# Kernel tuning notes

Hardware: AMD Instinct MI355X
Metric: run time of the kernel (lower is better)

## Reference

```python
import jax, jax.numpy as jnp
import numpy as np

TIME_STEPS = 49      # time_steps init arg
NUM_STEPS = 5000     # (time_steps+1)/dt = max_solve_steps
DT = 0.01            # dt0 in diffeqsolve
B = 8192             # batch of independent simulations


def setup_inputs() -> dict:
    key = jax.random.key(0)
    k1, k2, k3 = jax.random.split(key, 3)
    # positive, well-conditioned rates in [0.05, 0.5)
    condition = 0.05 + 0.45 * jax.random.uniform(k1, (B, 4), dtype=jnp.float32)
    # standard normals; scaled by sqrt(dt) inside reference -> Brownian increments
    dW = jax.random.normal(k2, (NUM_STEPS, B), dtype=jnp.float32)
    # uniform jitter used in summarize()'s max_at
    u = jax.random.uniform(k3, (B,), dtype=jnp.float32)
    return {"condition": condition, "dW": dW, "u": u}


def _simulate(condition, dW):
    # condition columns: infection_rate, recovery_rate, r0_mean_reversion, r0_volatility
    inf_rate = condition[:, 0]
    rec = condition[:, 1]
    mr = condition[:, 2]
    vol = condition[:, 3]
    r0_init = inf_rate / rec
    b = condition.shape[0]
    y0 = jnp.stack([
        jnp.full((b,), 0.99, condition.dtype),  # S
        jnp.full((b,), 0.01, condition.dtype),  # I
        jnp.zeros((b,), condition.dtype),       # R
        r0_init,                                # R0
    ], axis=-1)  # [B,4]
    sqrt_dt = jnp.sqrt(jnp.asarray(DT, condition.dtype))

    def step(y, dw):
        s, i, r, r0 = y[:, 0], y[:, 1], y[:, 2], y[:, 3]
        newly_infected = r0 * rec * s
        newly_recovered = rec * i
        # Euler-Maruyama: drift * dt + diffusion * dW, diffusion only on R0,
        # scaled by sqrt(|R0|) as in sde()
        y_new = jnp.stack([
            s - DT * newly_infected,
            i + DT * (newly_infected - newly_recovered),
            r + DT * newly_recovered,
            r0 + DT * mr * (r0_init - r0) + jnp.sqrt(jnp.abs(r0)) * vol * (dw * sqrt_dt),
        ], axis=-1)
        return y_new, y_new[:, 1]  # carry full state, emit infected fraction

    _, infected = jax.lax.scan(step, y0, dW)  # infected: [NUM_STEPS, B]
    # SaveAt ts = 1..TIME_STEPS: step k ends at t=(k+1)*DT, so t=m is index 100*m-1
    x = infected[99:100 * TIME_STEPS:100]  # [TIME_STEPS, B]
    return jnp.nan_to_num(x, nan=0.0, posinf=0.0, neginf=0.0)


def reference(condition, dW, u):
    x = _simulate(condition, dW)          # [T, B] infected trajectories
    x = jnp.clip(x, 1e-5)
    max_ = x.max(axis=0)
    max_at = (jnp.argmax(x, axis=0).astype(x.dtype) + u) / TIME_STEPS
    vol = jnp.std(jnp.diff(jnp.log(x), axis=0), axis=0)
    return jnp.stack([max_, max_at, vol], axis=-1)  # [B, 3]
```

## Files before the change

kernel.cpp:

```cpp
#include <hip/hip_runtime.h>
#include <math.h>

#define BATCH 8192
#define TPB   32
#define SLOT  100
#define NSLOT 49
#define RING  3
#define SLOT_BYTES  (SLOT * TPB * 4)
#define GROUP_BYTES (10 * TPB * 4)


__device__ __forceinline__ unsigned lds_addr_of(void* p) {
    return (unsigned)(unsigned long long)(__attribute__((address_space(3))) void*)p;
}

#define REP10(M) M(0) M(1) M(2) M(3) M(4) M(5) M(6) M(7) M(8) M(9)

#define DECLA(k) float A##k = 0.0f;
#define DECLB(k) float B##k = 0.0f;

#define DS_READ10(P, addr) asm volatile( \
    "ds_read_b32 %[d0], %[a] offset:0\n\t" \
    "ds_read_b32 %[d1], %[a] offset:128\n\t" \
    "ds_read_b32 %[d2], %[a] offset:256\n\t" \
    "ds_read_b32 %[d3], %[a] offset:384\n\t" \
    "ds_read_b32 %[d4], %[a] offset:512\n\t" \
    "ds_read_b32 %[d5], %[a] offset:640\n\t" \
    "ds_read_b32 %[d6], %[a] offset:768\n\t" \
    "ds_read_b32 %[d7], %[a] offset:896\n\t" \
    "ds_read_b32 %[d8], %[a] offset:1024\n\t" \
    "ds_read_b32 %[d9], %[a] offset:1152" \
    : [d0] "=v"(P##0), [d1] "=v"(P##1), [d2] "=v"(P##2), [d3] "=v"(P##3), \
      [d4] "=v"(P##4), [d5] "=v"(P##5), [d6] "=v"(P##6), [d7] "=v"(P##7), \
      [d8] "=v"(P##8), [d9] "=v"(P##9) \
    : [a] "v"(addr))

#define WAIT10(P) asm volatile("s_waitcnt lgkmcnt(10)" \
    : "+v"(P##0), "+v"(P##1), "+v"(P##2), "+v"(P##3), "+v"(P##4), \
      "+v"(P##5), "+v"(P##6), "+v"(P##7), "+v"(P##8), "+v"(P##9))

#define WAIT10_0(P) asm volatile("s_waitcnt lgkmcnt(0)" \
    : "+v"(P##0), "+v"(P##1), "+v"(P##2), "+v"(P##3), "+v"(P##4), \
      "+v"(P##5), "+v"(P##6), "+v"(P##7), "+v"(P##8), "+v"(P##9))

#define STEP_BODY(dwv) { \
    float dw  = (dwv); \
    float pr  = dtrec * r0; \
    float ps  = pr * s; \
    float r0a = r0 * c1 + c2; \
    float sq  = sqrtf(fabsf(r0)); \
    float g   = dw * volc; \
    s  = s - ps; \
    i_ = i_ * ci + ps; \
    r0 = r0a + sq * g; }

#define STEPA(k) STEP_BODY(A##k)
#define STEPB(k) STEP_BODY(B##k)

#define ISSUE_SLOT(kk) do { \
    const float* g_ = gp + (size_t)(kk) * (SLOT * BATCH); \
    float* l_ = &ring[(kk) % RING][0][0]; \
    _Pragma("unroll") \
    for (int ii = 0; ii < 25; ++ii) { \
        __builtin_amdgcn_global_load_lds( \
            (__attribute__((address_space(1))) void*)(g_), \
            (__attribute__((address_space(3))) void*)(l_), 16, 0, 0); \
        g_ += 4 * BATCH; \
        l_ += 4 * TPB; \
    } \
} while (0)

__global__ __launch_bounds__(TPB, 1)
void sir_sde_kernel(const float* __restrict__ cond,
                    const float* __restrict__ dW,
                    const float* __restrict__ uu,
                    float* __restrict__ out)
{
    __shared__ float ring[RING][SLOT][TPB];

    const int t = threadIdx.x;
    const int b = blockIdx.x * TPB + t;
    const int b0 = blockIdx.x * TPB;

    const float inf_rate = cond[b * 4 + 0];
    const float rec      = cond[b * 4 + 1];
    const float mr       = cond[b * 4 + 2];
    const float vol      = cond[b * 4 + 3];
    const float u        = uu[b];

    const float dt    = 0.01f;
    const float r0i   = inf_rate / rec;
    const float dtrec = dt * rec;
    const float ci    = 1.0f - dtrec;
    const float c1    = 1.0f - dt * mr;
    const float c2    = (dt * mr) * r0i;
    const float volc  = vol * sqrtf(dt);

    float s  = 0.99f;
    float i_ = 0.01f;
    float r0 = r0i;

    float maxv = -1.0f, maxat = 0.0f;
    float prevlx = 0.0f, sum = 0.0f, sumsq = 0.0f;

    REP10(DECLA)
    REP10(DECLB)

    const float* gp = dW + (size_t)(t >> 3) * BATCH + (size_t)(b0 + (t & 7) * 4);

    const unsigned ring_base = lds_addr_of(&ring[0][0][0]) + (unsigned)t * 4u;

    asm volatile("" ::: "memory");

    ISSUE_SLOT(0);
    ISSUE_SLOT(1);

#pragma unroll 1
    for (int k = 0; k < NSLOT; ++k) {
        if (k + 1 < NSLOT) { asm volatile("s_waitcnt vmcnt(25)"); }
        else               { asm volatile("s_waitcnt vmcnt(0)"); }

        if (k + 2 < NSLOT) ISSUE_SLOT(k + 2);

        unsigned a = ring_base + (unsigned)((k % RING) * SLOT_BYTES);

        DS_READ10(A, a); a += GROUP_BYTES;
        DS_READ10(B, a); a += GROUP_BYTES; WAIT10(A); REP10(STEPA)
        DS_READ10(A, a); a += GROUP_BYTES; WAIT10(B); REP10(STEPB)
        DS_READ10(B, a); a += GROUP_BYTES; WAIT10(A); REP10(STEPA)
        DS_READ10(A, a); a += GROUP_BYTES; WAIT10(B); REP10(STEPB)
        DS_READ10(B, a); a += GROUP_BYTES; WAIT10(A); REP10(STEPA)
        DS_READ10(A, a); a += GROUP_BYTES; WAIT10(B); REP10(STEPB)
        DS_READ10(B, a); a += GROUP_BYTES; WAIT10(A); REP10(STEPA)
        DS_READ10(A, a); a += GROUP_BYTES; WAIT10(B); REP10(STEPB)
        DS_READ10(B, a);                   WAIT10(A); REP10(STEPA)
                                           WAIT10_0(B); REP10(STEPB)

        {
            float x = __builtin_isfinite(i_) ? i_ : 0.0f;
            x = fmaxf(x, 1e-5f);
            float lx = logf(x);
            if (k > 0) {
                float d = lx - prevlx;
                sum   += d;
                sumsq += d * d;
            }
            prevlx = lx;
            if (x > maxv) { maxv = x; maxat = (float)k; }
        }
    }

    asm volatile("s_waitcnt vmcnt(0) lgkmcnt(0)" ::: "memory");

    float mean = sum / 48.0f;
    float var  = sumsq / 48.0f - mean * mean;
    var = fmaxf(var, 0.0f);
    float volout    = sqrtf(var);
    float maxat_out = (maxat + u) / 49.0f;

    out[b * 3 + 0] = maxv;
    out[b * 3 + 1] = maxat_out;
    out[b * 3 + 2] = volout;
}

extern "C" void kernel_launch(void* const* d_in, const int* in_sizes, int n_in,
                              void* d_out, int out_size, void* d_ws, size_t ws_size,
                              hipStream_t stream)
{
    (void)in_sizes; (void)n_in; (void)out_size; (void)d_ws; (void)ws_size;
    const float* cond = (const float*)d_in[0];
    const float* dW   = (const float*)d_in[1];
    const float* uu   = (const float*)d_in[2];
    float* out = (float*)d_out;

    dim3 grid(BATCH / TPB), block(TPB);
    hipLaunchKernelGGL(sir_sde_kernel, grid, block, 0, stream, cond, dW, uu, out);
}
```

Baseline: 563.4 us.

## Spread eight simulations per wave, loading dW into registers and broadcasting via shuffles

Replaces the half-wave, one-simulation-per-thread design that staged dW through an LDS ring. Each 64-lane block now owns 8 simulations. Each lane loads one dword per 8-step chunk straight into a register, keeping 8 loads in flight, and the values are broadcast across lanes with __shfl. The goal is to occupy all four SIMDs of each CU and keep more memory requests outstanding, removing the LDS staging and ds_read latency. In exchange every lane recomputes its column's recurrence redundantly, adds a shuffle per step, runs a few extra tail steps, and loads dW rows slightly past the needed range.

```diff
diff --git a/kernel.cpp b/kernel.cpp
--- a/kernel.cpp
+++ b/kernel.cpp
@@ -2,46 +2,11 @@
 #include <math.h>
 
 #define BATCH 8192
-#define TPB   32
-#define SLOT  100
-#define NSLOT 49
-#define RING  3
-#define SLOT_BYTES  (SLOT * TPB * 4)
-#define GROUP_BYTES (10 * TPB * 4)
+#define TPB   64
+#define COLS  8
+#define NBLK  (BATCH / COLS)
+#define CHUNK_BYTES 262144u
 
-
-__device__ __forceinline__ unsigned lds_addr_of(void* p) {
-    return (unsigned)(unsigned long long)(__attribute__((address_space(3))) void*)p;
-}
-
-#define REP10(M) M(0) M(1) M(2) M(3) M(4) M(5) M(6) M(7) M(8) M(9)
-
-#define DECLA(k) float A##k = 0.0f;
-#define DECLB(k) float B##k = 0.0f;
-
-#define DS_READ10(P, addr) asm volatile( \
-    "ds_read_b32 %[d0], %[a] offset:0\n\t" \
-    "ds_read_b32 %[d1], %[a] offset:128\n\t" \
-    "ds_read_b32 %[d2], %[a] offset:256\n\t" \
-    "ds_read_b32 %[d3], %[a] offset:384\n\t" \
-    "ds_read_b32 %[d4], %[a] offset:512\n\t" \
-    "ds_read_b32 %[d5], %[a] offset:640\n\t" \
-    "ds_read_b32 %[d6], %[a] offset:768\n\t" \
-    "ds_read_b32 %[d7], %[a] offset:896\n\t" \
-    "ds_read_b32 %[d8], %[a] offset:1024\n\t" \
-    "ds_read_b32 %[d9], %[a] offset:1152" \
-    : [d0] "=v"(P##0), [d1] "=v"(P##1), [d2] "=v"(P##2), [d3] "=v"(P##3), \
-      [d4] "=v"(P##4), [d5] "=v"(P##5), [d6] "=v"(P##6), [d7] "=v"(P##7), \
-      [d8] "=v"(P##8), [d9] "=v"(P##9) \
-    : [a] "v"(addr))
-
-#define WAIT10(P) asm volatile("s_waitcnt lgkmcnt(10)" \
-    : "+v"(P##0), "+v"(P##1), "+v"(P##2), "+v"(P##3), "+v"(P##4), \
-      "+v"(P##5), "+v"(P##6), "+v"(P##7), "+v"(P##8), "+v"(P##9))
-
-#define WAIT10_0(P) asm volatile("s_waitcnt lgkmcnt(0)" \
-    : "+v"(P##0), "+v"(P##1), "+v"(P##2), "+v"(P##3), "+v"(P##4), \
-      "+v"(P##5), "+v"(P##6), "+v"(P##7), "+v"(P##8), "+v"(P##9))
 
 #define STEP_BODY(dwv) { \
     float dw  = (dwv); \
@@ -54,20 +19,33 @@
     i_ = i_ * ci + ps; \
     r0 = r0a + sq * g; }
 
-#define STEPA(k) STEP_BODY(A##k)
-#define STEPB(k) STEP_BODY(B##k)
+#define ISSUE(Rr, cc) asm volatile( \
+    "global_load_dword %[d], %[o], %[sb]" \
+    : [d] "=v"(Rr) \
+    : [o] "v"(lane_off + (unsigned)(cc) * CHUNK_BYTES), [sb] "s"(dW))
 
-#define ISSUE_SLOT(kk) do { \
-    const float* g_ = gp + (size_t)(kk) * (SLOT * BATCH); \
-    float* l_ = &ring[(kk) % RING][0][0]; \
+#define WAIT7(Rr) asm volatile("s_waitcnt vmcnt(7)" : "+v"(Rr))
+
+#define RECORD(xx) { \
+    float x = __builtin_isfinite(xx) ? (xx) : 0.0f; \
+    x = fmaxf(x, 1e-5f); \
+    float lx = logf(x); \
+    if (reccount > 0) { float d = lx - prevlx; sum += d; sumsq += d * d; } \
+    prevlx = lx; \
+    if (x > maxv) { maxv = x; maxat = (float)reccount; } \
+    ++reccount; }
+
+#define CONSUME(Rr, cidx) do { \
+    WAIT7(Rr); \
+    const int hit = next_rec - ((cidx) << 3); \
+    float x_rec = 0.0f; \
     _Pragma("unroll") \
-    for (int ii = 0; ii < 25; ++ii) { \
-        __builtin_amdgcn_global_load_lds( \
-            (__attribute__((address_space(1))) void*)(g_), \
-            (__attribute__((address_space(3))) void*)(l_), 16, 0, 0); \
-        g_ += 4 * BATCH; \
-        l_ += 4 * TPB; \
+    for (int j = 0; j < 8; ++j) { \
+        float dwv = __shfl(Rr, (j << 3) + c, 64); \
+        STEP_BODY(dwv) \
+        if (j == hit) x_rec = i_; \
     } \
+    if (hit >= 0 && hit < 8) { RECORD(x_rec); next_rec += 100; } \
 } while (0)
 
 __global__ __launch_bounds__(TPB, 1)
@@ -76,11 +54,9 @@
                     const float* __restrict__ uu,
                     float* __restrict__ out)
 {
-    __shared__ float ring[RING][SLOT][TPB];
-
-    const int t = threadIdx.x;
-    const int b = blockIdx.x * TPB + t;
-    const int b0 = blockIdx.x * TPB;
+    const int l = threadIdx.x;
+    const int c = l & 7;
+    const int b = blockIdx.x * COLS + c;
 
     const float inf_rate = cond[b * 4 + 0];
     const float rec      = cond[b * 4 + 1];
@@ -102,55 +78,35 @@
 
     float maxv = -1.0f, maxat = 0.0f;
     float prevlx = 0.0f, sum = 0.0f, sumsq = 0.0f;
+    int   reccount = 0;
+    int   next_rec = 99;
 
-    REP10(DECLA)
-    REP10(DECLB)
+    const unsigned lane_off =
+        ((unsigned)(l >> 3) * (unsigned)BATCH
+         + (unsigned)blockIdx.x * (unsigned)COLS + (unsigned)c) * 4u;
 
-    const float* gp = dW + (size_t)(t >> 3) * BATCH + (size_t)(b0 + (t & 7) * 4);
+    float R0 = 0.0f, R1 = 0.0f, R2 = 0.0f, R3 = 0.0f;
+    float R4 = 0.0f, R5 = 0.0f, R6 = 0.0f, R7 = 0.0f;
 
-    const unsigned ring_base = lds_addr_of(&ring[0][0][0]) + (unsigned)t * 4u;
+    asm volatile("s_waitcnt vmcnt(0)" ::: "memory");
 
-    asm volatile("" ::: "memory");
-
-    ISSUE_SLOT(0);
-    ISSUE_SLOT(1);
+    ISSUE(R0, 0); ISSUE(R1, 1); ISSUE(R2, 2); ISSUE(R3, 3);
+    ISSUE(R4, 4); ISSUE(R5, 5); ISSUE(R6, 6); ISSUE(R7, 7);
 
 #pragma unroll 1
-    for (int k = 0; k < NSLOT; ++k) {
-        if (k + 1 < NSLOT) { asm volatile("s_waitcnt vmcnt(25)"); }
-        else               { asm volatile("s_waitcnt vmcnt(0)"); }
-
-        if (k + 2 < NSLOT) ISSUE_SLOT(k + 2);
-
-        unsigned a = ring_base + (unsigned)((k % RING) * SLOT_BYTES);
-
-        DS_READ10(A, a); a += GROUP_BYTES;
-        DS_READ10(B, a); a += GROUP_BYTES; WAIT10(A); REP10(STEPA)
-        DS_READ10(A, a); a += GROUP_BYTES; WAIT10(B); REP10(STEPB)
-        DS_READ10(B, a); a += GROUP_BYTES; WAIT10(A); REP10(STEPA)
-        DS_READ10(A, a); a += GROUP_BYTES; WAIT10(B); REP10(STEPB)
-        DS_READ10(B, a); a += GROUP_BYTES; WAIT10(A); REP10(STEPA)
-        DS_READ10(A, a); a += GROUP_BYTES; WAIT10(B); REP10(STEPB)
-        DS_READ10(B, a); a += GROUP_BYTES; WAIT10(A); REP10(STEPA)
-        DS_READ10(A, a); a += GROUP_BYTES; WAIT10(B); REP10(STEPB)
-        DS_READ10(B, a);                   WAIT10(A); REP10(STEPA)
-                                           WAIT10_0(B); REP10(STEPB)
-
-        {
-            float x = __builtin_isfinite(i_) ? i_ : 0.0f;
-            x = fmaxf(x, 1e-5f);
-            float lx = logf(x);
-            if (k > 0) {
-                float d = lx - prevlx;
-                sum   += d;
-                sumsq += d * d;
-            }
-            prevlx = lx;
-            if (x > maxv) { maxv = x; maxat = (float)k; }
-        }
+    for (int it = 0; it < 77; ++it) {
+        const int cb = it << 3;
+        CONSUME(R0, cb + 0); ISSUE(R0, cb + 8);
+        CONSUME(R1, cb + 1); ISSUE(R1, cb + 9);
+        CONSUME(R2, cb + 2); ISSUE(R2, cb + 10);
+        CONSUME(R3, cb + 3); ISSUE(R3, cb + 11);
+        CONSUME(R4, cb + 4); ISSUE(R4, cb + 12);
+        CONSUME(R5, cb + 5); ISSUE(R5, cb + 13);
+        CONSUME(R6, cb + 6); ISSUE(R6, cb + 14);
+        CONSUME(R7, cb + 7); ISSUE(R7, cb + 15);
     }
 
-    asm volatile("s_waitcnt vmcnt(0) lgkmcnt(0)" ::: "memory");
+    asm volatile("s_waitcnt vmcnt(0)" ::: "memory");
 
     float mean = sum / 48.0f;
     float var  = sumsq / 48.0f - mean * mean;
@@ -158,9 +114,11 @@
     float volout    = sqrtf(var);
     float maxat_out = (maxat + u) / 49.0f;
 
-    out[b * 3 + 0] = maxv;
-    out[b * 3 + 1] = maxat_out;
-    out[b * 3 + 2] = volout;
+    if (l < 8) {
+        out[b * 3 + 0] = maxv;
+        out[b * 3 + 1] = maxat_out;
+        out[b * 3 + 2] = volout;
+    }
 }
 
 extern "C" void kernel_launch(void* const* d_in, const int* in_sizes, int n_in,
@@ -173,6 +131,6 @@
     const float* uu   = (const float*)d_in[2];
     float* out = (float*)d_out;
 
-    dim3 grid(BATCH / TPB), block(TPB);
+    dim3 grid(NBLK), block(TPB);
     hipLaunchKernelGGL(sir_sde_kernel, grid, block, 0, stream, cond, dW, uu, out);
 }
```

New measurement: 521.7 us. 1.08x faster.
